# Performance work log

Hardware: AMD Instinct MI355X
Metric: run time of the kernel (lower is better)

## Reference

```python
import jax, jax.numpy as jnp
import numpy as np
import math

NUM_HEADS = 16
HEAD_DIM = 32  # latent_dim // num_heads = 512 // 16


def rope(x, pos):
    # x: (B, H, S, Dh); half-split rotary embedding, theta=10000
    d = x.shape[-1] // 2
    inv_freq = 1.0 / (10000.0 ** (jnp.arange(d, dtype=jnp.float32) / d))
    ang = pos.astype(jnp.float32)[:, None] * inv_freq[None, :]  # (S, d)
    cos, sin = jnp.cos(ang), jnp.sin(ang)
    x1, x2 = x[..., :d], x[..., d:]
    return jnp.concatenate([x1 * cos - x2 * sin, x1 * sin + x2 * cos], axis=-1)


def setup_inputs() -> dict:
    key = jax.random.key(0)
    ks = jax.random.split(key, 16)
    B, L, KV_PREV = 1, 2048, 2048
    D, D_KV = 2048, 512
    s = lambda fan_in: 1.0 / math.sqrt(fan_in)
    return {
        "x": jax.random.normal(ks[0], (B, L, D), jnp.float32),
        "z_cache": jax.random.normal(ks[1], (B, KV_PREV, D_KV), jnp.float32),
        "valid_lens": jax.random.randint(ks[2], (B, L), 1, KV_PREV + L, jnp.int32),
        "W_latent": jax.random.normal(ks[3], (D, D_KV), jnp.float32) * s(D),
        "b_latent": jnp.zeros((D_KV,), jnp.float32),
        "W_q": jax.random.normal(ks[4], (D, NUM_HEADS * HEAD_DIM), jnp.float32) * s(D),
        "b_q": jnp.zeros((NUM_HEADS * HEAD_DIM,), jnp.float32),
        "W_k": jax.random.normal(ks[5], (D_KV, NUM_HEADS * HEAD_DIM), jnp.float32) * s(D_KV),
        "b_k": jnp.zeros((NUM_HEADS * HEAD_DIM,), jnp.float32),
        "W_v": jax.random.normal(ks[6], (D_KV, NUM_HEADS * HEAD_DIM), jnp.float32) * s(D_KV),
        "b_v": jnp.zeros((NUM_HEADS * HEAD_DIM,), jnp.float32),
        "W_o": jax.random.normal(ks[7], (NUM_HEADS * HEAD_DIM, D), jnp.float32) * s(NUM_HEADS * HEAD_DIM),
        "b_o": jnp.zeros((D,), jnp.float32),
    }


def reference(x, z_cache, valid_lens, W_latent, b_latent, W_q, b_q, W_k, b_k, W_v, b_v, W_o, b_o):
    B, L, D = x.shape
    H, Dh = NUM_HEADS, HEAD_DIM
    # latent projection + cache concat
    z_new = x @ W_latent + b_latent                      # (B, L, D_kv)
    z = jnp.concatenate([z_cache, z_new], axis=1)        # (B, KV, D_kv)
    KV = z.shape[1]
    q = (x @ W_q + b_q).reshape(B, L, H, Dh).transpose(0, 2, 1, 3)   # (B,H,L,Dh)
    k = (z @ W_k + b_k).reshape(B, KV, H, Dh).transpose(0, 2, 1, 3)  # (B,H,KV,Dh)
    v = (z @ W_v + b_v).reshape(B, KV, H, Dh).transpose(0, 2, 1, 3)  # (B,H,KV,Dh)
    q = rope(q, jnp.arange(L))
    k = rope(k, jnp.arange(KV))
    scores = jnp.einsum("bhqd,bhkd->bhqk", q, k) / math.sqrt(Dh)     # (B,H,L,KV)
    # faithful: unmasked softmax (returned as attn_weights), then re-masked softmax
    attn_weights = jax.nn.softmax(scores, axis=-1)
    invalid = jnp.arange(KV)[None, None, None, :] >= valid_lens[:, None, :, None]
    masked = jnp.where(invalid, jnp.float32(-10000.0), scores)
    masked_w = jax.nn.softmax(masked, axis=-1)
    heads = jnp.einsum("bhqk,bhkd->bhqd", masked_w, v)               # (B,H,L,Dh)
    heads = heads.transpose(0, 2, 1, 3).reshape(B, L, H * Dh)
    output = heads @ W_o + b_o                                       # (B, L, D)
    return (output, z, attn_weights, scores)
```

## Files before the change

### kernel.cpp

```cpp
#include <hip/hip_runtime.h>
#include <math.h>

#define L_Q     2048
#define KV_PREV 2048
#define KV_TOT  4096
#define DIM     2048
#define D_KV    512
#define NH      16
#define DH      32
#define HDh     512
#define KC      256

typedef short bf16x8 __attribute__((ext_vector_type(8)));
typedef short bf16x4 __attribute__((ext_vector_type(4)));
typedef float f32x4  __attribute__((ext_vector_type(4)));

__device__ inline short f2bf(float f) {
    unsigned u = __float_as_uint(f);
    u += 0x7fff + ((u >> 16) & 1);
    return (short)(u >> 16);
}

__device__ __constant__ double c_invfreq[16] = {
    1.0, 0.5623413251903491, 0.31622776601683794, 0.17782794100389228,
    0.1, 0.05623413251903491, 0.03162277660168379, 0.017782794100389228,
    0.01, 0.005623413251903491, 0.0031622776601683794, 0.0017782794100389228,
    0.001, 0.0005623413251903491, 0.00031622776601683794, 0.00017782794100389227,
};

__global__ void cvt_bf16(const float* __restrict__ in, short* __restrict__ out, int n8) {
    int i = blockIdx.x * blockDim.x + threadIdx.x;
    if (i >= n8) return;
    float4 a = reinterpret_cast<const float4*>(in)[2 * i];
    float4 b = reinterpret_cast<const float4*>(in)[2 * i + 1];
    union { short s[8]; int4 v; } u;
    u.s[0] = f2bf(a.x); u.s[1] = f2bf(a.y); u.s[2] = f2bf(a.z); u.s[3] = f2bf(a.w);
    u.s[4] = f2bf(b.x); u.s[5] = f2bf(b.y); u.s[6] = f2bf(b.z); u.s[7] = f2bf(b.w);
    reinterpret_cast<int4*>(out)[i] = u.v;
}

__global__ void cvt_copy(const float* __restrict__ src, float* __restrict__ dst,
                         short* __restrict__ dbf, int n8) {
    int i = blockIdx.x * blockDim.x + threadIdx.x;
    if (i >= n8) return;
    float4 a = reinterpret_cast<const float4*>(src)[2 * i];
    float4 b = reinterpret_cast<const float4*>(src)[2 * i + 1];
    reinterpret_cast<float4*>(dst)[2 * i]     = a;
    reinterpret_cast<float4*>(dst)[2 * i + 1] = b;
    union { short s[8]; int4 v; } u;
    u.s[0] = f2bf(a.x); u.s[1] = f2bf(a.y); u.s[2] = f2bf(a.z); u.s[3] = f2bf(a.w);
    u.s[4] = f2bf(b.x); u.s[5] = f2bf(b.y); u.s[6] = f2bf(b.z); u.s[7] = f2bf(b.w);
    reinterpret_cast<int4*>(dbf)[i] = u.v;
}

__global__ __launch_bounds__(256) void tr_cvt(const float* __restrict__ in,
        short* __restrict__ out, int K, int N) {
    __shared__ float tile[32][33];
    int k0 = blockIdx.x * 32, n0 = blockIdx.y * 32;
    int c = threadIdx.x & 31, r0 = threadIdx.x >> 5;
    for (int r = r0; r < 32; r += 8)
        tile[r][c] = in[(size_t)(k0 + r) * N + n0 + c];
    __syncthreads();
    for (int r = r0; r < 32; r += 8)
        out[(size_t)(n0 + r) * K + k0 + c] = f2bf(tile[c][r]);
}

__global__ __launch_bounds__(256) void vt_cvt(const short* __restrict__ v, short* __restrict__ vt) {
    __shared__ short tile[64][34];
    int h = blockIdx.y, kv0 = blockIdx.x * 64;
    int c = threadIdx.x & 31, r0 = threadIdx.x >> 5;
    for (int r = r0; r < 64; r += 8)
        tile[r][c] = v[(size_t)(kv0 + r) * HDh + h * DH + c];
    __syncthreads();
    int l = threadIdx.x & 63, wv = threadIdx.x >> 6;
    for (int d = wv; d < 32; d += 4)
        vt[((size_t)h * DH + d) * KV_TOT + kv0 + l] = tile[l][d];
}

__global__ __launch_bounds__(256) void gemm_bf16(const short* __restrict__ A,
        const short* __restrict__ Bt, const float* __restrict__ bias,
        float* __restrict__ C, short* __restrict__ Cbf, int rope,
        int M, int N, int K)
{
    int t = threadIdx.x, w = t >> 6, l = t & 63, lr = l & 15, lg = l >> 4;
    int m0 = blockIdx.y * 64 + w * 16;
    int n0 = blockIdx.x * 64;
    f32x4 acc[4] = {{0,0,0,0},{0,0,0,0},{0,0,0,0},{0,0,0,0}};
    const short* ap  = A  + (size_t)(m0 + lr) * K + lg * 8;
    const short* bp0 = Bt + (size_t)(n0 + lr) * K + lg * 8;
    #pragma unroll 2
    for (int k0 = 0; k0 < K; k0 += 32) {
        bf16x8 a = *reinterpret_cast<const bf16x8*>(ap + k0);
        #pragma unroll
        for (int j = 0; j < 4; ++j) {
            bf16x8 b = *reinterpret_cast<const bf16x8*>(bp0 + (size_t)j * 16 * K + k0);
            acc[j] = __builtin_amdgcn_mfma_f32_16x16x32_bf16(a, b, acc[j], 0, 0, 0);
        }
    }
    float bs[4];
    #pragma unroll
    for (int j = 0; j < 4; ++j) bs[j] = bias[n0 + j * 16 + lr];

    if (rope) {
        #pragma unroll
        for (int r = 0; r < 4; ++r) {
            int m = m0 + lg * 4 + r;
            float ang = (float)((double)m * c_invfreq[lr]);
            float cs = cosf(ang), sn = sinf(ang);
            size_t rb = (size_t)m * N + n0 + lr;
            float a1 = acc[0][r] + bs[0], a2 = acc[1][r] + bs[1];
            Cbf[rb]      = f2bf(a1 * cs - a2 * sn);
            Cbf[rb + 16] = f2bf(a1 * sn + a2 * cs);
            float b1 = acc[2][r] + bs[2], b2 = acc[3][r] + bs[3];
            Cbf[rb + 32] = f2bf(b1 * cs - b2 * sn);
            Cbf[rb + 48] = f2bf(b1 * sn + b2 * cs);
        }
        return;
    }
    #pragma unroll
    for (int j = 0; j < 4; ++j) {
        int n = n0 + j * 16 + lr;
        #pragma unroll
        for (int r = 0; r < 4; ++r) {
            float v = acc[j][r] + bs[j];
            size_t idx = (size_t)(m0 + lg * 4 + r) * N + n;
            if (C)   C[idx] = v;
            if (Cbf) Cbf[idx] = f2bf(v);
        }
    }
}

__global__ __launch_bounds__(256) void scores_stats(const short* __restrict__ q,
        const short* __restrict__ kmat, const int* __restrict__ vlens,
        float* __restrict__ scores, float* __restrict__ isu_o, float* __restrict__ is2_o)
{
    __shared__ float Sl[4][16][KC + 4];
    int t = threadIdx.x, w = t >> 6, l = t & 63, lr = l & 15, lg = l >> 4;
    int h = blockIdx.y;
    int qrow = blockIdx.x * 64 + w * 16;
    int myq = qrow + lr;
    bf16x8 bQ = *reinterpret_cast<const bf16x8*>(q + (size_t)myq * HDh + h * DH + lg * 8);
    int vl = vlens[myq];
    const short* kp = kmat + h * DH + lg * 8;
    const float sc = 0.17677669529663687f;
    float su = 0.f, s2 = 0.f;
    const int kb = lg * 4;

    bf16x8 a0 = *reinterpret_cast<const bf16x8*>(kp + (size_t)lr * HDh);
    bf16x8 a1 = *reinterpret_cast<const bf16x8*>(kp + (size_t)(16 + lr) * HDh);
    for (int c = 0; c < KV_TOT / KC; ++c) {
        #pragma unroll
        for (int kt = 0; kt < KC / 32; ++kt) {
            int k0 = c * KC + kt * 32;
            int kn = (k0 + 32) & (KV_TOT - 1);
            bf16x8 a0n = *reinterpret_cast<const bf16x8*>(kp + (size_t)(kn + lr) * HDh);
            bf16x8 a1n = *reinterpret_cast<const bf16x8*>(kp + (size_t)(kn + 16 + lr) * HDh);
            f32x4 z4 = {0.f, 0.f, 0.f, 0.f};
            f32x4 s0 = __builtin_amdgcn_mfma_f32_16x16x32_bf16(a0, bQ, z4, 0, 0, 0);
            f32x4 s1 = __builtin_amdgcn_mfma_f32_16x16x32_bf16(a1, bQ, z4, 0, 0, 0);
            f32x4 o0, o1;
            #pragma unroll
            for (int r = 0; r < 4; ++r) { o0[r] = s0[r] * sc; o1[r] = s1[r] * sc; }
            *reinterpret_cast<f32x4*>(&Sl[w][lr][kt * 32 + kb])      = o0;
            *reinterpret_cast<f32x4*>(&Sl[w][lr][kt * 32 + 16 + kb]) = o1;
            #pragma unroll
            for (int r = 0; r < 4; ++r) {
                float e0 = __expf(o0[r]), e1 = __expf(o1[r]);
                su += e0 + e1;
                if (k0 + kb + r < vl)      s2 += e0;
                if (k0 + 16 + kb + r < vl) s2 += e1;
            }
            a0 = a0n; a1 = a1n;
        }
        #pragma unroll
        for (int r = 0; r < 16; ++r) {
            f32x4 v = *reinterpret_cast<const f32x4*>(&Sl[w][r][l * 4]);
            float* dst = scores + ((size_t)h * L_Q + qrow + r) * KV_TOT + c * KC + l * 4;
            __builtin_nontemporal_store(v, reinterpret_cast<f32x4*>(dst));
        }
    }
    su += __shfl_xor(su, 16, 64); su += __shfl_xor(su, 32, 64);
    s2 += __shfl_xor(s2, 16, 64); s2 += __shfl_xor(s2, 32, 64);
    if (lg == 0) {
        size_t idx = (size_t)h * L_Q + myq;
        isu_o[idx] = 1.f / su;
        is2_o[idx] = 1.f / s2;
    }
}

__global__ __launch_bounds__(256) void attn_pv(const short* __restrict__ q,
        const short* __restrict__ kmat, const int* __restrict__ vlens,
        const float* __restrict__ isu_i, const float* __restrict__ is2_i,
        const short* __restrict__ Vt,
        float* __restrict__ attn, short* __restrict__ heads_bf)
{
    __shared__ float Al[4][16][KC + 4];
    __shared__ short Plds[4][16][72];
    int t = threadIdx.x, w = t >> 6, l = t & 63, lr = l & 15, lg = l >> 4;
    int h = blockIdx.y;
    int qrow = blockIdx.x * 64 + w * 16;
    int myq = qrow + lr;
    bf16x8 bQ = *reinterpret_cast<const bf16x8*>(q + (size_t)myq * HDh + h * DH + lg * 8);
    int vl = vlens[myq];
    size_t sidx = (size_t)h * L_Q + myq;
    float isu = isu_i[sidx], is2 = is2_i[sidx];
    const short* kp  = kmat + h * DH + lg * 8;
    const short* vp0 = Vt + ((size_t)h * DH + lr) * KV_TOT + lg * 8;
    const short* vp1 = vp0 + (size_t)16 * KV_TOT;
    const float sc = 0.17677669529663687f;
    short* prow = &Plds[w][lr][0];
    f32x4 h0 = {0,0,0,0}, h1 = {0,0,0,0};

    for (int c = 0; c < KV_TOT / KC; ++c) {
        #pragma unroll
        for (int g = 0; g < KC / 64; ++g) {
            #pragma unroll
            for (int kt = 0; kt < 4; ++kt) {
                int kk = c * KC + g * 64 + kt * 16;
                bf16x8 aK = *reinterpret_cast<const bf16x8*>(kp + (size_t)(kk + lr) * HDh);
                f32x4 z4 = {0.f, 0.f, 0.f, 0.f};
                f32x4 s = __builtin_amdgcn_mfma_f32_16x16x32_bf16(aK, bQ, z4, 0, 0, 0);
                f32x4 oa;
                bf16x4 pb;
                #pragma unroll
                for (int r = 0; r < 4; ++r) {
                    float e = __expf(s[r] * sc);
                    oa[r] = e * isu;
                    pb[r] = (kk + lg * 4 + r < vl) ? f2bf(e * is2) : (short)0;
                }
                *reinterpret_cast<f32x4*>(&Al[w][lr][g * 64 + kt * 16 + lg * 4]) = oa;
                *reinterpret_cast<bf16x4*>(prow + kt * 16 + lg * 4) = pb;
            }
            #pragma unroll
            for (int kbl = 0; kbl < 2; ++kbl) {
                int kv = c * KC + g * 64 + kbl * 32;
                bf16x8 pa = *reinterpret_cast<const bf16x8*>(prow + kbl * 32 + lg * 8);
                bf16x8 b0 = *reinterpret_cast<const bf16x8*>(vp0 + kv);
                bf16x8 b1 = *reinterpret_cast<const bf16x8*>(vp1 + kv);
                h0 = __builtin_amdgcn_mfma_f32_16x16x32_bf16(pa, b0, h0, 0, 0, 0);
                h1 = __builtin_amdgcn_mfma_f32_16x16x32_bf16(pa, b1, h1, 0, 0, 0);
            }
        }
        #pragma unroll
        for (int r = 0; r < 16; ++r) {
            f32x4 v = *reinterpret_cast<const f32x4*>(&Al[w][r][l * 4]);
            float* dst = attn + ((size_t)h * L_Q + qrow + r) * KV_TOT + c * KC + l * 4;
            __builtin_nontemporal_store(v, reinterpret_cast<f32x4*>(dst));
        }
    }
    #pragma unroll
    for (int r = 0; r < 4; ++r) {
        size_t ho = (size_t)(qrow + lg * 4 + r) * HDh + h * DH + lr;
        heads_bf[ho]      = f2bf(h0[r]);
        heads_bf[ho + 16] = f2bf(h1[r]);
    }
}

extern "C" void kernel_launch(void* const* d_in, const int* in_sizes, int n_in,
                              void* d_out, int out_size, void* d_ws, size_t ws_size,
                              hipStream_t stream) {
    const float* x       = (const float*)d_in[0];
    const float* z_cache = (const float*)d_in[1];
    const int*   vlens   = (const int*)  d_in[2];
    const float* W_lat   = (const float*)d_in[3];
    const float* b_lat   = (const float*)d_in[4];
    const float* W_q     = (const float*)d_in[5];
    const float* b_q     = (const float*)d_in[6];
    const float* W_k     = (const float*)d_in[7];
    const float* b_k     = (const float*)d_in[8];
    const float* W_v     = (const float*)d_in[9];
    const float* b_v     = (const float*)d_in[10];
    const float* W_o     = (const float*)d_in[11];
    const float* b_o     = (const float*)d_in[12];

    float* out        = (float*)d_out;
    float* out_output = out;
    float* out_z      = out_output + (size_t)L_Q * DIM;
    float* out_attn   = out_z + (size_t)KV_TOT * D_KV;
    float* out_scores = out_attn + (size_t)NH * L_Q * KV_TOT;

    float* wf     = (float*)d_ws;
    float* ws_isu = wf;
    float* ws_is2 = ws_isu + (size_t)NH * L_Q;
    short* wsb      = (short*)(ws_is2 + (size_t)NH * L_Q);
    short* x_bf     = wsb;
    short* z_bf     = x_bf + (size_t)L_Q * DIM;
    short* q_bf     = z_bf + (size_t)KV_TOT * D_KV;
    short* k_bf     = q_bf + (size_t)L_Q * HDh;
    short* v_bf     = k_bf + (size_t)KV_TOT * HDh;
    short* Vt       = v_bf + (size_t)KV_TOT * HDh;
    short* heads_bf = Vt + (size_t)NH * DH * KV_TOT;
    short* Wt_lat   = heads_bf + (size_t)L_Q * HDh;
    short* Wt_q     = Wt_lat + (size_t)D_KV * DIM;
    short* Wt_k     = Wt_q + (size_t)HDh * DIM;
    short* Wt_v     = Wt_k + (size_t)HDh * D_KV;
    short* Wt_o     = Wt_v + (size_t)HDh * D_KV;

    cvt_bf16<<<(L_Q * DIM / 8 + 255) / 256, 256, 0, stream>>>(x, x_bf, L_Q * DIM / 8);
    cvt_copy<<<(KV_PREV * D_KV / 8 + 255) / 256, 256, 0, stream>>>(
        z_cache, out_z, z_bf, KV_PREV * D_KV / 8);
    tr_cvt<<<dim3(DIM / 32, D_KV / 32), 256, 0, stream>>>(W_lat, Wt_lat, DIM, D_KV);
    tr_cvt<<<dim3(DIM / 32, HDh / 32), 256, 0, stream>>>(W_q, Wt_q, DIM, HDh);
    tr_cvt<<<dim3(D_KV / 32, HDh / 32), 256, 0, stream>>>(W_k, Wt_k, D_KV, HDh);
    tr_cvt<<<dim3(D_KV / 32, HDh / 32), 256, 0, stream>>>(W_v, Wt_v, D_KV, HDh);
    tr_cvt<<<dim3(HDh / 32, DIM / 32), 256, 0, stream>>>(W_o, Wt_o, HDh, DIM);

    gemm_bf16<<<dim3(D_KV / 64, L_Q / 64), 256, 0, stream>>>(
        x_bf, Wt_lat, b_lat, out_z + (size_t)KV_PREV * D_KV,
        z_bf + (size_t)KV_PREV * D_KV, 0, L_Q, D_KV, DIM);

    gemm_bf16<<<dim3(HDh / 64, L_Q / 64), 256, 0, stream>>>(
        x_bf, Wt_q, b_q, nullptr, q_bf, 1, L_Q, HDh, DIM);
    gemm_bf16<<<dim3(HDh / 64, KV_TOT / 64), 256, 0, stream>>>(
        z_bf, Wt_k, b_k, nullptr, k_bf, 1, KV_TOT, HDh, D_KV);
    gemm_bf16<<<dim3(HDh / 64, KV_TOT / 64), 256, 0, stream>>>(
        z_bf, Wt_v, b_v, nullptr, v_bf, 0, KV_TOT, HDh, D_KV);
    vt_cvt<<<dim3(KV_TOT / 64, NH), 256, 0, stream>>>(v_bf, Vt);

    scores_stats<<<dim3(L_Q / 64, NH), 256, 0, stream>>>(
        q_bf, k_bf, vlens, out_scores, ws_isu, ws_is2);

    attn_pv<<<dim3(L_Q / 64, NH), 256, 0, stream>>>(
        q_bf, k_bf, vlens, ws_isu, ws_is2, Vt, out_attn, heads_bf);

    gemm_bf16<<<dim3(DIM / 64, L_Q / 64), 256, 0, stream>>>(
        heads_bf, Wt_o, b_o, out_output, nullptr, 0, L_Q, DIM, HDh);
}
```

Before: 560.1 us.

## Split KV across two waves per block, stage scores in bf16, merge weight transposes

The five weight-transpose launches are merged into one kernel. The two attention kernels now run 128-thread blocks of two waves, each covering one 16-query tile and half of the KV range. Blocks are remapped with an XCD-style swizzle, and the two halves' softmax sums and PV partials are combined through shared memory. Scores and attention weights are staged in LDS as bf16 and widened back to fp32 on store, and the masked softmax is recovered by rescaling the unmasked weights. This cuts LDS use and raises parallelism, but the stored scores and attn_weights outputs lose precision to bf16 and the nontemporal stores are dropped.

New measurement: 645.7 us. 15.3% more time.

```diff
diff --git a/kernel.cpp b/kernel.cpp
--- a/kernel.cpp
+++ b/kernel.cpp
@@ -53,10 +53,22 @@
     reinterpret_cast<int4*>(dbf)[i] = u.v;
 }
 
-__global__ __launch_bounds__(256) void tr_cvt(const float* __restrict__ in,
-        short* __restrict__ out, int K, int N) {
+__global__ __launch_bounds__(256) void tr_cvt_all(
+        const float* __restrict__ W0, const float* __restrict__ W1,
+        const float* __restrict__ W2, const float* __restrict__ W3,
+        const float* __restrict__ W4,
+        short* __restrict__ O0, short* __restrict__ O1, short* __restrict__ O2,
+        short* __restrict__ O3, short* __restrict__ O4) {
     __shared__ float tile[32][33];
-    int k0 = blockIdx.x * 32, n0 = blockIdx.y * 32;
+    int b = blockIdx.x;
+    const float* in; short* out; int K, N;
+    if (b < 1024)      { in = W0; out = O0; K = 2048; N = 512; }
+    else if (b < 2048) { in = W1; out = O1; K = 2048; N = 512;  b -= 1024; }
+    else if (b < 2304) { in = W2; out = O2; K = 512;  N = 512;  b -= 2048; }
+    else if (b < 2560) { in = W3; out = O3; K = 512;  N = 512;  b -= 2304; }
+    else               { in = W4; out = O4; K = 512;  N = 2048; b -= 2560; }
+    int nkb = K / 32;
+    int k0 = (b % nkb) * 32, n0 = (b / nkb) * 32;
     int c = threadIdx.x & 31, r0 = threadIdx.x >> 5;
     for (int r = r0; r < 32; r += 8)
         tile[r][c] = in[(size_t)(k0 + r) * N + n0 + c];
@@ -130,14 +142,17 @@
     }
 }
 
-__global__ __launch_bounds__(256) void scores_stats(const short* __restrict__ q,
+__global__ __launch_bounds__(128) void scores_stats(const short* __restrict__ q,
         const short* __restrict__ kmat, const int* __restrict__ vlens,
         float* __restrict__ scores, float* __restrict__ isu_o, float* __restrict__ is2_o)
 {
-    __shared__ float Sl[4][16][KC + 4];
+    __shared__ __align__(16) short Sl[2][16][KC + 8];
+    __shared__ float red[2][16][2];
     int t = threadIdx.x, w = t >> 6, l = t & 63, lr = l & 15, lg = l >> 4;
-    int h = blockIdx.y;
-    int qrow = blockIdx.x * 64 + w * 16;
+    int bid = (int)blockIdx.x;
+    int sbid = (bid & 7) * 256 + (bid >> 3);
+    int h = sbid >> 7, qb = sbid & 127;
+    int qrow = qb * 16;
     int myq = qrow + lr;
     bf16x8 bQ = *reinterpret_cast<const bf16x8*>(q + (size_t)myq * HDh + h * DH + lg * 8);
     int vl = vlens[myq];
@@ -145,114 +160,137 @@
     const float sc = 0.17677669529663687f;
     float su = 0.f, s2 = 0.f;
     const int kb = lg * 4;
-
-    bf16x8 a0 = *reinterpret_cast<const bf16x8*>(kp + (size_t)lr * HDh);
-    bf16x8 a1 = *reinterpret_cast<const bf16x8*>(kp + (size_t)(16 + lr) * HDh);
-    for (int c = 0; c < KV_TOT / KC; ++c) {
-        #pragma unroll
-        for (int kt = 0; kt < KC / 32; ++kt) {
-            int k0 = c * KC + kt * 32;
-            int kn = (k0 + 32) & (KV_TOT - 1);
-            bf16x8 a0n = *reinterpret_cast<const bf16x8*>(kp + (size_t)(kn + lr) * HDh);
-            bf16x8 a1n = *reinterpret_cast<const bf16x8*>(kp + (size_t)(kn + 16 + lr) * HDh);
+    const int khalf = w * (KV_TOT / 2);
+
+    for (int c = 0; c < KV_TOT / (2 * KC); ++c) {
+        int kbase = khalf + c * KC;
+        #pragma unroll
+        for (int i = 0; i < 16; ++i) {
+            bf16x8 aK = *reinterpret_cast<const bf16x8*>(kp + (size_t)(kbase + i * 16 + lr) * HDh);
             f32x4 z4 = {0.f, 0.f, 0.f, 0.f};
-            f32x4 s0 = __builtin_amdgcn_mfma_f32_16x16x32_bf16(a0, bQ, z4, 0, 0, 0);
-            f32x4 s1 = __builtin_amdgcn_mfma_f32_16x16x32_bf16(a1, bQ, z4, 0, 0, 0);
-            f32x4 o0, o1;
-            #pragma unroll
-            for (int r = 0; r < 4; ++r) { o0[r] = s0[r] * sc; o1[r] = s1[r] * sc; }
-            *reinterpret_cast<f32x4*>(&Sl[w][lr][kt * 32 + kb])      = o0;
-            *reinterpret_cast<f32x4*>(&Sl[w][lr][kt * 32 + 16 + kb]) = o1;
+            f32x4 s = __builtin_amdgcn_mfma_f32_16x16x32_bf16(aK, bQ, z4, 0, 0, 0);
+            bf16x4 sb4;
             #pragma unroll
             for (int r = 0; r < 4; ++r) {
-                float e0 = __expf(o0[r]), e1 = __expf(o1[r]);
-                su += e0 + e1;
-                if (k0 + kb + r < vl)      s2 += e0;
-                if (k0 + 16 + kb + r < vl) s2 += e1;
+                float v = s[r] * sc;
+                float e = __expf(v);
+                su += e;
+                if (kbase + i * 16 + kb + r < vl) s2 += e;
+                sb4[r] = f2bf(v);
             }
-            a0 = a0n; a1 = a1n;
+            *reinterpret_cast<bf16x4*>(&Sl[w][lr][i * 16 + kb]) = sb4;
         }
         #pragma unroll
         for (int r = 0; r < 16; ++r) {
-            f32x4 v = *reinterpret_cast<const f32x4*>(&Sl[w][r][l * 4]);
-            float* dst = scores + ((size_t)h * L_Q + qrow + r) * KV_TOT + c * KC + l * 4;
-            __builtin_nontemporal_store(v, reinterpret_cast<f32x4*>(dst));
+            ushort4 uv = *reinterpret_cast<const ushort4*>(&Sl[w][r][l * 4]);
+            f32x4 o;
+            o[0] = __uint_as_float((unsigned)uv.x << 16);
+            o[1] = __uint_as_float((unsigned)uv.y << 16);
+            o[2] = __uint_as_float((unsigned)uv.z << 16);
+            o[3] = __uint_as_float((unsigned)uv.w << 16);
+            *reinterpret_cast<f32x4*>(
+                scores + ((size_t)h * L_Q + qrow + r) * KV_TOT + kbase + l * 4) = o;
         }
     }
     su += __shfl_xor(su, 16, 64); su += __shfl_xor(su, 32, 64);
     s2 += __shfl_xor(s2, 16, 64); s2 += __shfl_xor(s2, 32, 64);
-    if (lg == 0) {
-        size_t idx = (size_t)h * L_Q + myq;
-        isu_o[idx] = 1.f / su;
-        is2_o[idx] = 1.f / s2;
-    }
-}
-
-__global__ __launch_bounds__(256) void attn_pv(const short* __restrict__ q,
+    if (lg == 0) { red[w][lr][0] = su; red[w][lr][1] = s2; }
+    __syncthreads();
+    if (t < 16) {
+        float sut = red[0][t][0] + red[1][t][0];
+        float s2t = red[0][t][1] + red[1][t][1];
+        size_t idx = (size_t)h * L_Q + qrow + t;
+        isu_o[idx] = 1.f / sut;
+        is2_o[idx] = 1.f / s2t;
+    }
+}
+
+__global__ __launch_bounds__(128) void attn_pv(const short* __restrict__ q,
         const short* __restrict__ kmat, const int* __restrict__ vlens,
         const float* __restrict__ isu_i, const float* __restrict__ is2_i,
         const short* __restrict__ Vt,
         float* __restrict__ attn, short* __restrict__ heads_bf)
 {
-    __shared__ float Al[4][16][KC + 4];
-    __shared__ short Plds[4][16][72];
+    __shared__ __align__(16) short Al[2][16][KC + 8];
+    __shared__ __align__(16) float hstage[64][8];
     int t = threadIdx.x, w = t >> 6, l = t & 63, lr = l & 15, lg = l >> 4;
-    int h = blockIdx.y;
-    int qrow = blockIdx.x * 64 + w * 16;
+    int bid = (int)blockIdx.x;
+    int sbid = (bid & 7) * 256 + (bid >> 3);
+    int h = sbid >> 7, qb = sbid & 127;
+    int qrow = qb * 16;
     int myq = qrow + lr;
     bf16x8 bQ = *reinterpret_cast<const bf16x8*>(q + (size_t)myq * HDh + h * DH + lg * 8);
     int vl = vlens[myq];
     size_t sidx = (size_t)h * L_Q + myq;
-    float isu = isu_i[sidx], is2 = is2_i[sidx];
+    float isu = isu_i[sidx];
     const short* kp  = kmat + h * DH + lg * 8;
     const short* vp0 = Vt + ((size_t)h * DH + lr) * KV_TOT + lg * 8;
     const short* vp1 = vp0 + (size_t)16 * KV_TOT;
     const float sc = 0.17677669529663687f;
-    short* prow = &Plds[w][lr][0];
+    const int kb = lg * 4;
+    const int khalf = w * (KV_TOT / 2);
     f32x4 h0 = {0,0,0,0}, h1 = {0,0,0,0};
 
-    for (int c = 0; c < KV_TOT / KC; ++c) {
-        #pragma unroll
-        for (int g = 0; g < KC / 64; ++g) {
+    for (int c = 0; c < KV_TOT / (2 * KC); ++c) {
+        int kbase = khalf + c * KC;
+        #pragma unroll
+        for (int g = 0; g < 4; ++g) {
             #pragma unroll
             for (int kt = 0; kt < 4; ++kt) {
-                int kk = c * KC + g * 64 + kt * 16;
-                bf16x8 aK = *reinterpret_cast<const bf16x8*>(kp + (size_t)(kk + lr) * HDh);
+                int i = g * 4 + kt;
+                bf16x8 aK = *reinterpret_cast<const bf16x8*>(
+                    kp + (size_t)(kbase + i * 16 + lr) * HDh);
                 f32x4 z4 = {0.f, 0.f, 0.f, 0.f};
                 f32x4 s = __builtin_amdgcn_mfma_f32_16x16x32_bf16(aK, bQ, z4, 0, 0, 0);
-                f32x4 oa;
-                bf16x4 pb;
+                bf16x4 ab4;
                 #pragma unroll
-                for (int r = 0; r < 4; ++r) {
-                    float e = __expf(s[r] * sc);
-                    oa[r] = e * isu;
-                    pb[r] = (kk + lg * 4 + r < vl) ? f2bf(e * is2) : (short)0;
-                }
-                *reinterpret_cast<f32x4*>(&Al[w][lr][g * 64 + kt * 16 + lg * 4]) = oa;
-                *reinterpret_cast<bf16x4*>(prow + kt * 16 + lg * 4) = pb;
+                for (int r = 0; r < 4; ++r)
+                    ab4[r] = f2bf(__expf(s[r] * sc) * isu);
+                *reinterpret_cast<bf16x4*>(&Al[w][lr][i * 16 + kb]) = ab4;
             }
             #pragma unroll
             for (int kbl = 0; kbl < 2; ++kbl) {
-                int kv = c * KC + g * 64 + kbl * 32;
-                bf16x8 pa = *reinterpret_cast<const bf16x8*>(prow + kbl * 32 + lg * 8);
-                bf16x8 b0 = *reinterpret_cast<const bf16x8*>(vp0 + kv);
-                bf16x8 b1 = *reinterpret_cast<const bf16x8*>(vp1 + kv);
+                int koff = g * 64 + kbl * 32;
+                bf16x8 raw = *reinterpret_cast<const bf16x8*>(&Al[w][lr][koff + lg * 8]);
+                bf16x8 pa;
+                #pragma unroll
+                for (int j = 0; j < 8; ++j)
+                    pa[j] = (kbase + koff + lg * 8 + j < vl) ? raw[j] : (short)0;
+                bf16x8 b0 = *reinterpret_cast<const bf16x8*>(vp0 + kbase + koff);
+                bf16x8 b1 = *reinterpret_cast<const bf16x8*>(vp1 + kbase + koff);
                 h0 = __builtin_amdgcn_mfma_f32_16x16x32_bf16(pa, b0, h0, 0, 0, 0);
                 h1 = __builtin_amdgcn_mfma_f32_16x16x32_bf16(pa, b1, h1, 0, 0, 0);
             }
         }
         #pragma unroll
         for (int r = 0; r < 16; ++r) {
-            f32x4 v = *reinterpret_cast<const f32x4*>(&Al[w][r][l * 4]);
-            float* dst = attn + ((size_t)h * L_Q + qrow + r) * KV_TOT + c * KC + l * 4;
-            __builtin_nontemporal_store(v, reinterpret_cast<f32x4*>(dst));
-        }
-    }
-    #pragma unroll
-    for (int r = 0; r < 4; ++r) {
-        size_t ho = (size_t)(qrow + lg * 4 + r) * HDh + h * DH + lr;
-        heads_bf[ho]      = f2bf(h0[r]);
-        heads_bf[ho + 16] = f2bf(h1[r]);
+            ushort4 uv = *reinterpret_cast<const ushort4*>(&Al[w][r][l * 4]);
+            f32x4 o;
+            o[0] = __uint_as_float((unsigned)uv.x << 16);
+            o[1] = __uint_as_float((unsigned)uv.y << 16);
+            o[2] = __uint_as_float((unsigned)uv.z << 16);
+            o[3] = __uint_as_float((unsigned)uv.w << 16);
+            *reinterpret_cast<f32x4*>(
+                attn + ((size_t)h * L_Q + qrow + r) * KV_TOT + kbase + l * 4) = o;
+        }
+    }
+    if (w == 1) {
+        *reinterpret_cast<f32x4*>(&hstage[l][0]) = h0;
+        *reinterpret_cast<f32x4*>(&hstage[l][4]) = h1;
+    }
+    __syncthreads();
+    if (w == 0) {
+        f32x4 g0 = *reinterpret_cast<const f32x4*>(&hstage[l][0]);
+        f32x4 g1 = *reinterpret_cast<const f32x4*>(&hstage[l][4]);
+        #pragma unroll
+        for (int r = 0; r < 4; ++r) {
+            int q2 = qrow + lg * 4 + r;
+            size_t i2 = (size_t)h * L_Q + q2;
+            float cc = is2_i[i2] / isu_i[i2];
+            size_t ho = (size_t)q2 * HDh + h * DH + lr;
+            heads_bf[ho]      = f2bf((h0[r] + g0[r]) * cc);
+            heads_bf[ho + 16] = f2bf((h1[r] + g1[r]) * cc);
+        }
     }
 }
 
@@ -299,11 +337,8 @@
     cvt_bf16<<<(L_Q * DIM / 8 + 255) / 256, 256, 0, stream>>>(x, x_bf, L_Q * DIM / 8);
     cvt_copy<<<(KV_PREV * D_KV / 8 + 255) / 256, 256, 0, stream>>>(
         z_cache, out_z, z_bf, KV_PREV * D_KV / 8);
-    tr_cvt<<<dim3(DIM / 32, D_KV / 32), 256, 0, stream>>>(W_lat, Wt_lat, DIM, D_KV);
-    tr_cvt<<<dim3(DIM / 32, HDh / 32), 256, 0, stream>>>(W_q, Wt_q, DIM, HDh);
-    tr_cvt<<<dim3(D_KV / 32, HDh / 32), 256, 0, stream>>>(W_k, Wt_k, D_KV, HDh);
-    tr_cvt<<<dim3(D_KV / 32, HDh / 32), 256, 0, stream>>>(W_v, Wt_v, D_KV, HDh);
-    tr_cvt<<<dim3(HDh / 32, DIM / 32), 256, 0, stream>>>(W_o, Wt_o, HDh, DIM);
+    tr_cvt_all<<<3584, 256, 0, stream>>>(W_lat, W_q, W_k, W_v, W_o,
+                                         Wt_lat, Wt_q, Wt_k, Wt_v, Wt_o);
 
     gemm_bf16<<<dim3(D_KV / 64, L_Q / 64), 256, 0, stream>>>(
         x_bf, Wt_lat, b_lat, out_z + (size_t)KV_PREV * D_KV,
@@ -317,10 +352,10 @@
         z_bf, Wt_v, b_v, nullptr, v_bf, 0, KV_TOT, HDh, D_KV);
     vt_cvt<<<dim3(KV_TOT / 64, NH), 256, 0, stream>>>(v_bf, Vt);
 
-    scores_stats<<<dim3(L_Q / 64, NH), 256, 0, stream>>>(
+    scores_stats<<<2048, 128, 0, stream>>>(
         q_bf, k_bf, vlens, out_scores, ws_isu, ws_is2);
 
-    attn_pv<<<dim3(L_Q / 64, NH), 256, 0, stream>>>(
+    attn_pv<<<2048, 128, 0, stream>>>(
         q_bf, k_bf, vlens, ws_isu, ws_is2, Vt, out_attn, heads_bf);
 
     gemm_bf16<<<dim3(DIM / 64, L_Q / 64), 256, 0, stream>>>(
```
